# Performance work log

Measured on AMD Instinct MI355X. Metric: run time of the kernel, lower is better.

The kernel has to match this reference:

```python
import jax, jax.numpy as jnp
import numpy as np

B, S, D_IN, D_OUT = 4, 2048, 768, 768

def setup_inputs() -> dict:
    key = jax.random.key(0)
    kx, kq, kk, kv = jax.random.split(key, 4)
    scale = 1.0 / np.sqrt(D_IN)
    return {
        "x": jax.random.normal(kx, (B, S, D_IN), dtype=jnp.float32),
        "Wq": jax.random.normal(kq, (D_OUT, D_IN), dtype=jnp.float32) * scale,
        "Wk": jax.random.normal(kk, (D_OUT, D_IN), dtype=jnp.float32) * scale,
        "Wv": jax.random.normal(kv, (D_OUT, D_IN), dtype=jnp.float32) * scale,
    }

def reference(x, Wq, Wk, Wv):
    # torch Linear: y = x @ W.T  (W is [d_out, d_in])
    q = jnp.einsum('bsd,od->bso', x, Wq)
    k = jnp.einsum('bsd,od->bso', x, Wk)
    v = jnp.einsum('bsd,od->bso', x, Wv)
    scores = jnp.einsum('bqo,bko->bqk', q, k)  # [B,S,S]
    causal = jnp.tril(jnp.ones((scores.shape[1], scores.shape[2]), dtype=bool))
    neg_inf = jnp.array(-jnp.inf, dtype=scores.dtype)
    scores = jnp.where(causal, scores, neg_inf)
    inv_sqrt_d = jnp.asarray(1.0 / np.sqrt(q.shape[-1]), dtype=scores.dtype)
    weights = jax.nn.softmax(scores * inv_sqrt_d, axis=-1)
    # dropout p=0.0 -> identity
    return jnp.einsum('bqk,bko->bqo', weights, v)
```

## Files before the change

kernel.cpp:

```cpp
#include <hip/hip_runtime.h>
#include <hip/hip_bf16.h>
#include <cstdint>
#include <cstddef>


typedef __attribute__((ext_vector_type(8))) short short8;
typedef __attribute__((ext_vector_type(4))) float f32x4;

#define GPTR(p) (const __attribute__((address_space(1))) void*)(p)
#define LPTR(p) (__attribute__((address_space(3))) void*)(p)

constexpr int CB = 4, CS = 2048, CD = 768;
constexpr int CBS = CB * CS;

__device__ inline unsigned short f2bf_bits(float v) {
    __hip_bfloat16 h = __float2bfloat16(v);
    unsigned short u;
    __builtin_memcpy(&u, &h, 2);
    return u;
}

__device__ inline ushort4 cvt4(float4 f) {
    ushort4 u;
    u.x = f2bf_bits(f.x); u.y = f2bf_bits(f.y);
    u.z = f2bf_bits(f.z); u.w = f2bf_bits(f.w);
    return u;
}

__global__ __launch_bounds__(256) void cvt_all(
    const float4* __restrict__ x,  const float4* __restrict__ wq,
    const float4* __restrict__ wk, const float4* __restrict__ wv,
    ushort4* __restrict__ x16, ushort4* __restrict__ w16,
    float4* __restrict__ rsum4)
{
    constexpr int NX = CBS * CD / 4;
    constexpr int NW = CD * CD / 4;
    constexpr int NT = NX + 3 * NW;
    const int i = blockIdx.x * 256 + threadIdx.x;
    if (i < NX) {
        x16[i] = cvt4(x[i]);
    } else if (i < NT) {
        const int j = i - NX;
        if (j < NW)            w16[j] = cvt4(wq[j]);
        else if (j < 2 * NW)   w16[j] = cvt4(wk[j - NW]);
        else                   w16[j] = cvt4(wv[j - 2 * NW]);
    } else {
        const int j = i - NT;
        rsum4[j] = float4{0.f, 0.f, 0.f, 0.f};
    }
}

template <int BM>
__device__ __forceinline__ void gemm_core(
    const __hip_bfloat16* __restrict__ A,
    const __hip_bfloat16* __restrict__ B,
    __hip_bfloat16* As, __hip_bfloat16* Bs,
    int m0, int n0, int K, int kend,
    f32x4 (&acc)[BM / 32][4])
{
    constexpr int AC = BM / 16;
    constexpr int SC = AC + 8;
    constexpr int MI = BM / 32;

    const int t  = threadIdx.x;
    const int w  = t >> 6;
    const int l  = t & 63;
    const int lq = l >> 4;
    const int lm = l & 15;
    const int wm = (w >> 1) * (BM / 2);
    const int wn = (w & 1) * 64;

    const int srow = l >> 2;
    const int scol = (l & 3) * 8;

    auto stage = [&](int buf, int k0) {
#pragma unroll
        for (int ci = 0; ci < SC / 4; ++ci) {
            const int c = ci * 4 + w;
            if (c < AC) {
                __builtin_amdgcn_global_load_lds(
                    GPTR(A + (size_t)(m0 + c * 16 + srow) * K + k0 + scol),
                    LPTR(&As[buf * BM * 32 + c * 512]), 16, 0, 0);
            } else {
                const int c2 = c - AC;
                __builtin_amdgcn_global_load_lds(
                    GPTR(B + (size_t)(n0 + c2 * 16 + srow) * K + k0 + scol),
                    LPTR(&Bs[buf * 128 * 32 + c2 * 512]), 16, 0, 0);
            }
        }
    };

    stage(0, 0);
    asm volatile("s_waitcnt vmcnt(0)");
    __syncthreads();

    int cur = 0;
    for (int k0 = 0; k0 < kend; k0 += 32) {
        if (k0 + 32 < kend)
            stage(cur ^ 1, k0 + 32);

        short8 af[MI], bf[4];
#pragma unroll
        for (int i = 0; i < MI; ++i)
            af[i] = *(const short8*)&As[cur * BM * 32 + (wm + i * 16 + lm) * 32 + lq * 8];
#pragma unroll
        for (int j = 0; j < 4; ++j)
            bf[j] = *(const short8*)&Bs[cur * 128 * 32 + (wn + j * 16 + lm) * 32 + lq * 8];

#pragma unroll
        for (int i = 0; i < MI; ++i)
#pragma unroll
            for (int j = 0; j < 4; ++j)
                acc[i][j] = __builtin_amdgcn_mfma_f32_16x16x32_bf16(
                    af[i], bf[j], acc[i][j], 0, 0, 0);

        __syncthreads();
        cur ^= 1;
    }
}

template <int MI>
__device__ __forceinline__ void zero_acc(f32x4 (&acc)[MI][4]) {
#pragma unroll
    for (int i = 0; i < MI; ++i)
#pragma unroll
        for (int j = 0; j < 4; ++j)
            acc[i][j] = f32x4{0.f, 0.f, 0.f, 0.f};
}

__global__ __launch_bounds__(256) void qkv_gemm(
    const __hip_bfloat16* __restrict__ x16,
    const __hip_bfloat16* __restrict__ w16,
    __hip_bfloat16* __restrict__ q16,
    __hip_bfloat16* __restrict__ k16,
    __hip_bfloat16* __restrict__ vt16)
{
    __shared__ __align__(16) __hip_bfloat16 As[2 * 128 * 32];
    __shared__ __align__(16) __hip_bfloat16 Bs[2 * 128 * 32];

    const int t  = threadIdx.x;
    const int w  = t >> 6;
    const int l  = t & 63;
    const int lq = l >> 4;
    const int lm = l & 15;
    const int wm = (w >> 1) * 64;
    const int wn = (w & 1) * 64;

    f32x4 acc[4][4];
    zero_acc<4>(acc);

    const __hip_bfloat16* A;
    const __hip_bfloat16* B;
    __hip_bfloat16* C;
    int m0, n0, ldc;

    const int id = blockIdx.x;
    if (id < 768) {
        const int proj = id / 384;
        const int r    = id % 384;
        n0 = (r % 6) * 128;
        m0 = (r / 6) * 128;
        A = x16; B = w16 + (size_t)proj * CD * CD;
        C = proj ? k16 : q16; ldc = CD;
    } else {
        int r = id - 768;
        const int b  = r / 96;  r %= 96;
        n0 = (r % 16) * 128;
        m0 = (r / 16) * 128;
        A = w16 + (size_t)2 * CD * CD;
        B = x16  + (size_t)b * CS * CD;
        C = vt16 + (size_t)b * CD * CS; ldc = CS;
    }

    gemm_core<128>(A, B, As, Bs, m0, n0, CD, CD, acc);

#pragma unroll
    for (int i = 0; i < 4; ++i)
#pragma unroll
        for (int j = 0; j < 4; ++j) {
            const int n = n0 + wn + j * 16 + lm;
#pragma unroll
            for (int r = 0; r < 4; ++r) {
                const int m = m0 + wm + i * 16 + lq * 4 + r;
                C[(size_t)m * ldc + n] = __float2bfloat16(acc[i][j][r]);
            }
        }
}

__global__ __launch_bounds__(256) void scores_gemm(
    const __hip_bfloat16* __restrict__ q16,
    const __hip_bfloat16* __restrict__ k16,
    __hip_bfloat16* __restrict__ sp16,
    float* __restrict__ rowsum,
    float scale)
{
    const int g  = blockIdx.x;
    const int b  = g & 3;
    const int tt = g >> 2;
    int s = (int)sqrtf((float)tt);
    while ((s + 1) * (s + 1) <= tt) ++s;
    while (s * s > tt) --s;
    int mi, nj;
    if (tt < s * (s + 1)) { mi = 2 * s - 1; nj = tt - s * s; }
    else                  { mi = 2 * s;     nj = tt - s * (s + 1); }
    const int m0 = mi * 64;
    const int n0 = nj * 128;

    __shared__ __align__(16) __hip_bfloat16 As[2 * 64 * 32];
    __shared__ __align__(16) __hip_bfloat16 Bs[2 * 128 * 32];

    const __hip_bfloat16* A = q16 + (size_t)b * CS * CD;
    const __hip_bfloat16* B = k16 + (size_t)b * CS * CD;
    __hip_bfloat16* C = sp16 + (size_t)b * CS * CS;
    float* rs = rowsum + (size_t)b * CS;

    f32x4 acc[2][4];
    zero_acc<2>(acc);
    gemm_core<64>(A, B, As, Bs, m0, n0, CD, CD, acc);

    const int t  = threadIdx.x;
    const int w  = t >> 6;
    const int l  = t & 63;
    const int lq = l >> 4;
    const int lm = l & 15;
    const int wm = (w >> 1) * 32;
    const int wn = (w & 1) * 64;

#pragma unroll
    for (int i = 0; i < 2; ++i) {
        float psum[4] = {0.f, 0.f, 0.f, 0.f};
#pragma unroll
        for (int j = 0; j < 4; ++j) {
            const int n = n0 + wn + j * 16 + lm;
#pragma unroll
            for (int r = 0; r < 4; ++r) {
                const int m = m0 + wm + i * 16 + lq * 4 + r;
                float e = (n <= m) ? __expf(acc[i][j][r] * scale) : 0.f;
                C[(size_t)m * CS + n] = __float2bfloat16(e);
                psum[r] += e;
            }
        }
#pragma unroll
        for (int r = 0; r < 4; ++r) {
#pragma unroll
            for (int off = 1; off < 16; off <<= 1)
                psum[r] += __shfl_xor(psum[r], off);
            if (lm == 0) {
                const int m = m0 + wm + i * 16 + lq * 4 + r;
                atomicAdd(&rs[m], psum[r]);
            }
        }
    }
}

__global__ __launch_bounds__(256) void pv_gemm(
    const __hip_bfloat16* __restrict__ sp16,
    const __hip_bfloat16* __restrict__ vt16,
    const float* __restrict__ rowsum,
    float* __restrict__ out)
{
    const int id   = blockIdx.x;
    const int mrev = id / 24;
    int r          = id % 24;
    const int b    = r / 6;
    const int n0   = (r % 6) * 128;
    const int mi   = 31 - mrev;
    const int m0   = mi * 64;
    const int kend = m0 + 64;

    __shared__ __align__(16) __hip_bfloat16 As[2 * 64 * 32];
    __shared__ __align__(16) __hip_bfloat16 Bs[2 * 128 * 32];

    const __hip_bfloat16* A = sp16 + (size_t)b * CS * CS;
    const __hip_bfloat16* B = vt16 + (size_t)b * CD * CS;
    float* Co = out + (size_t)b * CS * CD;
    const float* rs = rowsum + (size_t)b * CS;

    f32x4 acc[2][4];
    zero_acc<2>(acc);
    gemm_core<64>(A, B, As, Bs, m0, n0, CS, kend, acc);

    const int t  = threadIdx.x;
    const int w  = t >> 6;
    const int l  = t & 63;
    const int lq = l >> 4;
    const int lm = l & 15;
    const int wm = (w >> 1) * 32;
    const int wn = (w & 1) * 64;

#pragma unroll
    for (int i = 0; i < 2; ++i) {
        float inv[4];
#pragma unroll
        for (int r2 = 0; r2 < 4; ++r2)
            inv[r2] = 1.0f / rs[m0 + wm + i * 16 + lq * 4 + r2];
#pragma unroll
        for (int j = 0; j < 4; ++j) {
            const int n = n0 + wn + j * 16 + lm;
#pragma unroll
            for (int r2 = 0; r2 < 4; ++r2) {
                const int m = m0 + wm + i * 16 + lq * 4 + r2;
                Co[(size_t)m * CD + n] = acc[i][j][r2] * inv[r2];
            }
        }
    }
}

extern "C" void kernel_launch(void* const* d_in, const int* in_sizes, int n_in,
                              void* d_out, int out_size, void* d_ws, size_t ws_size,
                              hipStream_t stream)
{
    const float* x  = (const float*)d_in[0];
    const float* Wq = (const float*)d_in[1];
    const float* Wk = (const float*)d_in[2];
    const float* Wv = (const float*)d_in[3];
    float* out = (float*)d_out;

    char* ws = (char*)d_ws;
    size_t off = 0;
    auto alloc = [&](size_t bytes) { char* p = ws + off; off += bytes; return p; };

    __hip_bfloat16* x16  = (__hip_bfloat16*)alloc((size_t)CBS * CD * 2);
    __hip_bfloat16* q16  = (__hip_bfloat16*)alloc((size_t)CBS * CD * 2);
    __hip_bfloat16* k16  = (__hip_bfloat16*)alloc((size_t)CBS * CD * 2);
    __hip_bfloat16* vt16 = (__hip_bfloat16*)alloc((size_t)CBS * CD * 2);
    __hip_bfloat16* sp16 = (__hip_bfloat16*)alloc((size_t)CB * CS * CS * 2);
    __hip_bfloat16* w16  = (__hip_bfloat16*)alloc((size_t)3 * CD * CD * 2);
    float*          rsum = (float*)alloc((size_t)CB * CS * sizeof(float));

    constexpr int NCVT_BLK = (CBS * CD + 3 * CD * CD) / 4 / 256 + 8;
    cvt_all<<<NCVT_BLK, 256, 0, stream>>>(
        (const float4*)x, (const float4*)Wq, (const float4*)Wk, (const float4*)Wv,
        (ushort4*)x16, (ushort4*)w16, (float4*)rsum);

    qkv_gemm<<<1152, 256, 0, stream>>>(x16, w16, q16, k16, vt16);

    scores_gemm<<<1088, 256, 0, stream>>>(
        q16, k16, sp16, rsum, 0.03608439182435161f);

    pv_gemm<<<768, 256, 0, stream>>>(sp16, vt16, rsum, out);
}
```

Baseline: 193.9 us.

## Use 256x256 tiled 8-wave GEMM core and move V projection into scores launch

Replaces the 128-tile GEMM core with a 256x256 tile, 512-thread kernel that uses XOR-swizzled LDS, a staged per-quarter prefetch pipeline and priority-raised MFMA phases. The Q/K projections get their own kernel, and the V^T projection now runs in the same launch as the causal scores GEMM so the two fill the GPU together. The aim is more data reuse per tile and better overlap of loads with MFMA work. In exchange, grids are much smaller (192 and 240 blocks), which risks poor CU occupancy and tail imbalance, and the causal diagonal tiles waste more work at this tile size.

```diff
diff --git a/kernel.cpp b/kernel.cpp
--- a/kernel.cpp
+++ b/kernel.cpp
@@ -9,6 +9,7 @@
 
 #define GPTR(p) (const __attribute__((address_space(1))) void*)(p)
 #define LPTR(p) (__attribute__((address_space(3))) void*)(p)
+#define MFMA16(a8, b8, c) c = __builtin_amdgcn_mfma_f32_16x16x32_bf16(a8, b8, c, 0, 0, 0)
 
 constexpr int CB = 4, CS = 2048, CD = 768;
 constexpr int CBS = CB * CS;
@@ -25,6 +26,15 @@
     u.x = f2bf_bits(f.x); u.y = f2bf_bits(f.y);
     u.z = f2bf_bits(f.z); u.w = f2bf_bits(f.w);
     return u;
+}
+
+template <int MI>
+__device__ __forceinline__ void zero_acc(f32x4 (&acc)[MI][4]) {
+#pragma unroll
+    for (int i = 0; i < MI; ++i)
+#pragma unroll
+        for (int j = 0; j < 4; ++j)
+            acc[i][j] = f32x4{0.f, 0.f, 0.f, 0.f};
 }
 
 __global__ __launch_bounds__(256) void cvt_all(
@@ -50,6 +60,279 @@
     }
 }
 
+__device__ __forceinline__ void gemm256_core(
+    const __hip_bfloat16* __restrict__ A,
+    const __hip_bfloat16* __restrict__ B,
+    __hip_bfloat16* As, __hip_bfloat16* Bs,
+    int m0, int n0, int K, int nkt,
+    f32x4 (&acc)[8][4])
+{
+    const int t   = threadIdx.x;
+    const int w   = t >> 6;
+    const int l   = t & 63;
+    const int lq  = l >> 4;
+    const int lm  = l & 15;
+    const int wm  = w >> 2;
+    const int wn  = w & 3;
+    const int lm7 = lm & 7;
+    const int c0  = (lq ^ lm7) << 3;
+    const int c1  = c0 ^ 32;
+
+    const int rr0   = t >> 3;
+    const int gp8   = (t & 7) << 3;
+    const int g8    = (((t & 7) ^ (rr0 & 7)) << 3);
+    const int rowBa = ((rr0 & 32) << 1) | (rr0 & 31);
+
+    const __hip_bfloat16* Aori = A + (size_t)m0 * K;
+    const __hip_bfloat16* Bori = B + (size_t)n0 * K;
+
+    auto stage = [&](int reg, int bufT, int kt) {
+        const int kc = kt * 64 + g8;
+        const __hip_bfloat16* s0;
+        __hip_bfloat16* d;
+        if (reg == 0) {
+            s0 = Aori + (size_t)rr0 * K + kc;
+            d  = As + bufT * 16384 + rr0 * 64 + gp8;
+        } else if (reg == 2) {
+            s0 = Aori + (size_t)(64 + rr0) * K + kc;
+            d  = As + bufT * 16384 + (64 + rr0) * 64 + gp8;
+        } else if (reg == 3) {
+            s0 = Bori + (size_t)rowBa * K + kc;
+            d  = Bs + bufT * 16384 + rowBa * 64 + gp8;
+        } else {
+            s0 = Bori + (size_t)(32 + rowBa) * K + kc;
+            d  = Bs + bufT * 16384 + (32 + rowBa) * 64 + gp8;
+        }
+        __builtin_amdgcn_global_load_lds(GPTR(s0), LPTR(d), 16, 0, 0);
+        __builtin_amdgcn_global_load_lds(GPTR(s0 + (size_t)128 * K), LPTR(d + 8192), 16, 0, 0);
+    };
+
+    stage(0, 0, 0); stage(1, 0, 0); stage(2, 0, 0); stage(3, 0, 0);
+    stage(0, 1, 1); stage(1, 1, 1); stage(2, 1, 1);
+    asm volatile("s_waitcnt vmcnt(6)" ::: "memory");
+    __builtin_amdgcn_s_barrier();
+
+    for (int kt = 0; kt < nkt; ++kt) {
+        const int buf = kt & 1;
+        const __hip_bfloat16* Ab = As + buf * 16384 + wm * 8192 + lm * 64;
+        const __hip_bfloat16* Bb = Bs + buf * 16384 + (wn >> 1) * 8192 + (wn & 1) * 4096 + lm * 64;
+        short8 af[4][2], bf[2][2];
+
+#pragma unroll
+        for (int i = 0; i < 4; ++i) {
+            af[i][0] = *(const short8*)&Ab[i * 1024 + c0];
+            af[i][1] = *(const short8*)&Ab[i * 1024 + c1];
+        }
+#pragma unroll
+        for (int j = 0; j < 2; ++j) {
+            bf[j][0] = *(const short8*)&Bb[j * 1024 + c0];
+            bf[j][1] = *(const short8*)&Bb[j * 1024 + c1];
+        }
+        if (kt + 1 < nkt) stage(3, buf ^ 1, kt + 1);
+        __builtin_amdgcn_s_barrier();
+        asm volatile("s_waitcnt lgkmcnt(0)" ::: "memory");
+        __builtin_amdgcn_sched_barrier(0);
+        __builtin_amdgcn_s_setprio(1);
+#pragma unroll
+        for (int i = 0; i < 4; ++i)
+#pragma unroll
+            for (int j = 0; j < 2; ++j) {
+                MFMA16(af[i][0], bf[j][0], acc[i][j]);
+                MFMA16(af[i][1], bf[j][1], acc[i][j]);
+            }
+        __builtin_amdgcn_s_setprio(0);
+        __builtin_amdgcn_s_barrier();
+
+#pragma unroll
+        for (int j = 0; j < 2; ++j) {
+            bf[j][0] = *(const short8*)&Bb[(2 + j) * 1024 + c0];
+            bf[j][1] = *(const short8*)&Bb[(2 + j) * 1024 + c1];
+        }
+        if (kt + 2 < nkt) stage(0, buf, kt + 2);
+        __builtin_amdgcn_s_barrier();
+        asm volatile("s_waitcnt lgkmcnt(0)" ::: "memory");
+        __builtin_amdgcn_sched_barrier(0);
+        __builtin_amdgcn_s_setprio(1);
+#pragma unroll
+        for (int i = 0; i < 4; ++i)
+#pragma unroll
+            for (int j = 0; j < 2; ++j) {
+                MFMA16(af[i][0], bf[j][0], acc[i][2 + j]);
+                MFMA16(af[i][1], bf[j][1], acc[i][2 + j]);
+            }
+        __builtin_amdgcn_s_setprio(0);
+        __builtin_amdgcn_s_barrier();
+
+#pragma unroll
+        for (int i = 0; i < 4; ++i) {
+            af[i][0] = *(const short8*)&Ab[(4 + i) * 1024 + c0];
+            af[i][1] = *(const short8*)&Ab[(4 + i) * 1024 + c1];
+        }
+        if (kt + 2 < nkt) stage(1, buf, kt + 2);
+        __builtin_amdgcn_s_barrier();
+        asm volatile("s_waitcnt lgkmcnt(0)" ::: "memory");
+        __builtin_amdgcn_sched_barrier(0);
+        __builtin_amdgcn_s_setprio(1);
+#pragma unroll
+        for (int i = 0; i < 4; ++i)
+#pragma unroll
+            for (int j = 0; j < 2; ++j) {
+                MFMA16(af[i][0], bf[j][0], acc[4 + i][2 + j]);
+                MFMA16(af[i][1], bf[j][1], acc[4 + i][2 + j]);
+            }
+        __builtin_amdgcn_s_setprio(0);
+        __builtin_amdgcn_s_barrier();
+
+#pragma unroll
+        for (int j = 0; j < 2; ++j) {
+            bf[j][0] = *(const short8*)&Bb[j * 1024 + c0];
+            bf[j][1] = *(const short8*)&Bb[j * 1024 + c1];
+        }
+        if (kt + 2 < nkt) stage(2, buf, kt + 2);
+        __builtin_amdgcn_s_barrier();
+        asm volatile("s_waitcnt lgkmcnt(0)" ::: "memory");
+        __builtin_amdgcn_sched_barrier(0);
+        __builtin_amdgcn_s_setprio(1);
+#pragma unroll
+        for (int i = 0; i < 4; ++i)
+#pragma unroll
+            for (int j = 0; j < 2; ++j) {
+                MFMA16(af[i][0], bf[j][0], acc[4 + i][j]);
+                MFMA16(af[i][1], bf[j][1], acc[4 + i][j]);
+            }
+        __builtin_amdgcn_s_setprio(0);
+        if (kt + 2 < nkt) {
+            asm volatile("s_waitcnt vmcnt(6)" ::: "memory");
+        } else if (kt + 1 < nkt) {
+            asm volatile("s_waitcnt vmcnt(0)" ::: "memory");
+        }
+        __builtin_amdgcn_s_barrier();
+    }
+}
+
+__global__ __launch_bounds__(512, 2) void qk256_gemm(
+    const __hip_bfloat16* __restrict__ x16,
+    const __hip_bfloat16* __restrict__ w16,
+    __hip_bfloat16* __restrict__ q16,
+    __hip_bfloat16* __restrict__ k16)
+{
+    __shared__ __align__(16) __hip_bfloat16 As[2 * 16384];
+    __shared__ __align__(16) __hip_bfloat16 Bs[2 * 16384];
+
+    const int id   = blockIdx.x;
+    const int mi   = id / 6;
+    const int r    = id % 6;
+    const int proj = r / 3;
+    const int nj   = r % 3;
+    const int m0 = mi * 256, n0 = nj * 256;
+
+    f32x4 acc[8][4];
+    zero_acc<8>(acc);
+    gemm256_core(x16, w16 + (size_t)proj * CD * CD, As, Bs, m0, n0, CD, CD / 64, acc);
+
+    __hip_bfloat16* C = proj ? k16 : q16;
+    const int t = threadIdx.x, w = t >> 6, l = t & 63, lq = l >> 4, lm = l & 15;
+    const int wm = w >> 2, wn = w & 3;
+#pragma unroll
+    for (int i = 0; i < 8; ++i)
+#pragma unroll
+        for (int j = 0; j < 4; ++j) {
+            const int n = n0 + wn * 64 + j * 16 + lm;
+#pragma unroll
+            for (int r2 = 0; r2 < 4; ++r2) {
+                const int m = m0 + wm * 128 + i * 16 + lq * 4 + r2;
+                C[(size_t)m * CD + n] = __float2bfloat16(acc[i][j][r2]);
+            }
+        }
+}
+
+__global__ __launch_bounds__(512, 2) void scores_vt_gemm(
+    const __hip_bfloat16* __restrict__ q16,
+    const __hip_bfloat16* __restrict__ k16,
+    const __hip_bfloat16* __restrict__ x16,
+    const __hip_bfloat16* __restrict__ w16,
+    __hip_bfloat16* __restrict__ sp16,
+    __hip_bfloat16* __restrict__ vt16,
+    float* __restrict__ rowsum,
+    float scale)
+{
+    __shared__ __align__(16) __hip_bfloat16 As[2 * 16384];
+    __shared__ __align__(16) __hip_bfloat16 Bs[2 * 16384];
+
+    const int id = blockIdx.x;
+    const __hip_bfloat16 *A, *B;
+    int m0, n0, b;
+    const bool is_sc = (id < 144);
+    if (is_sc) {
+        b = id / 36;
+        const int tt = id % 36;
+        int mi = (int)((sqrtf(8.f * tt + 1.f) - 1.f) * 0.5f);
+        while ((mi + 1) * (mi + 2) / 2 <= tt) ++mi;
+        while (mi * (mi + 1) / 2 > tt) --mi;
+        const int nj = tt - mi * (mi + 1) / 2;
+        m0 = mi * 256; n0 = nj * 256;
+        A = q16 + (size_t)b * CS * CD;
+        B = k16 + (size_t)b * CS * CD;
+    } else {
+        int r = id - 144;
+        b = r / 24; r %= 24;
+        m0 = (r >> 3) * 256;
+        n0 = (r & 7) * 256;
+        A = w16 + (size_t)2 * CD * CD;
+        B = x16 + (size_t)b * CS * CD;
+    }
+
+    f32x4 acc[8][4];
+    zero_acc<8>(acc);
+    gemm256_core(A, B, As, Bs, m0, n0, CD, CD / 64, acc);
+
+    const int t = threadIdx.x, w = t >> 6, l = t & 63, lq = l >> 4, lm = l & 15;
+    const int wm = w >> 2, wn = w & 3;
+
+    if (is_sc) {
+        __hip_bfloat16* C = sp16 + (size_t)b * CS * CS;
+        float* rs = rowsum + (size_t)b * CS;
+#pragma unroll
+        for (int i = 0; i < 8; ++i) {
+            float psum[4] = {0.f, 0.f, 0.f, 0.f};
+#pragma unroll
+            for (int j = 0; j < 4; ++j) {
+                const int n = n0 + wn * 64 + j * 16 + lm;
+#pragma unroll
+                for (int r2 = 0; r2 < 4; ++r2) {
+                    const int m = m0 + wm * 128 + i * 16 + lq * 4 + r2;
+                    float e = (n <= m) ? __expf(acc[i][j][r2] * scale) : 0.f;
+                    C[(size_t)m * CS + n] = __float2bfloat16(e);
+                    psum[r2] += e;
+                }
+            }
+#pragma unroll
+            for (int r2 = 0; r2 < 4; ++r2) {
+#pragma unroll
+                for (int off = 1; off < 16; off <<= 1)
+                    psum[r2] += __shfl_xor(psum[r2], off);
+                if (lm == 0) {
+                    const int m = m0 + wm * 128 + i * 16 + lq * 4 + r2;
+                    atomicAdd(&rs[m], psum[r2]);
+                }
+            }
+        }
+    } else {
+        __hip_bfloat16* C = vt16 + (size_t)b * CD * CS;
+#pragma unroll
+        for (int i = 0; i < 8; ++i)
+#pragma unroll
+            for (int j = 0; j < 4; ++j) {
+                const int n = n0 + wn * 64 + j * 16 + lm;
+#pragma unroll
+                for (int r2 = 0; r2 < 4; ++r2) {
+                    const int m = m0 + wm * 128 + i * 16 + lq * 4 + r2;
+                    C[(size_t)m * CS + n] = __float2bfloat16(acc[i][j][r2]);
+                }
+            }
+    }
+}
+
 template <int BM>
 __device__ __forceinline__ void gemm_core(
     const __hip_bfloat16* __restrict__ A,
@@ -91,7 +374,7 @@
     };
 
     stage(0, 0);
-    asm volatile("s_waitcnt vmcnt(0)");
+    asm volatile("s_waitcnt vmcnt(0)" ::: "memory");
     __syncthreads();
 
     int cur = 0;
@@ -116,140 +399,6 @@
 
         __syncthreads();
         cur ^= 1;
-    }
-}
-
-template <int MI>
-__device__ __forceinline__ void zero_acc(f32x4 (&acc)[MI][4]) {
-#pragma unroll
-    for (int i = 0; i < MI; ++i)
-#pragma unroll
-        for (int j = 0; j < 4; ++j)
-            acc[i][j] = f32x4{0.f, 0.f, 0.f, 0.f};
-}
-
-__global__ __launch_bounds__(256) void qkv_gemm(
-    const __hip_bfloat16* __restrict__ x16,
-    const __hip_bfloat16* __restrict__ w16,
-    __hip_bfloat16* __restrict__ q16,
-    __hip_bfloat16* __restrict__ k16,
-    __hip_bfloat16* __restrict__ vt16)
-{
-    __shared__ __align__(16) __hip_bfloat16 As[2 * 128 * 32];
-    __shared__ __align__(16) __hip_bfloat16 Bs[2 * 128 * 32];
-
-    const int t  = threadIdx.x;
-    const int w  = t >> 6;
-    const int l  = t & 63;
-    const int lq = l >> 4;
-    const int lm = l & 15;
-    const int wm = (w >> 1) * 64;
-    const int wn = (w & 1) * 64;
-
-    f32x4 acc[4][4];
-    zero_acc<4>(acc);
-
-    const __hip_bfloat16* A;
-    const __hip_bfloat16* B;
-    __hip_bfloat16* C;
-    int m0, n0, ldc;
-
-    const int id = blockIdx.x;
-    if (id < 768) {
-        const int proj = id / 384;
-        const int r    = id % 384;
-        n0 = (r % 6) * 128;
-        m0 = (r / 6) * 128;
-        A = x16; B = w16 + (size_t)proj * CD * CD;
-        C = proj ? k16 : q16; ldc = CD;
-    } else {
-        int r = id - 768;
-        const int b  = r / 96;  r %= 96;
-        n0 = (r % 16) * 128;
-        m0 = (r / 16) * 128;
-        A = w16 + (size_t)2 * CD * CD;
-        B = x16  + (size_t)b * CS * CD;
-        C = vt16 + (size_t)b * CD * CS; ldc = CS;
-    }
-
-    gemm_core<128>(A, B, As, Bs, m0, n0, CD, CD, acc);
-
-#pragma unroll
-    for (int i = 0; i < 4; ++i)
-#pragma unroll
-        for (int j = 0; j < 4; ++j) {
-            const int n = n0 + wn + j * 16 + lm;
-#pragma unroll
-            for (int r = 0; r < 4; ++r) {
-                const int m = m0 + wm + i * 16 + lq * 4 + r;
-                C[(size_t)m * ldc + n] = __float2bfloat16(acc[i][j][r]);
-            }
-        }
-}
-
-__global__ __launch_bounds__(256) void scores_gemm(
-    const __hip_bfloat16* __restrict__ q16,
-    const __hip_bfloat16* __restrict__ k16,
-    __hip_bfloat16* __restrict__ sp16,
-    float* __restrict__ rowsum,
-    float scale)
-{
-    const int g  = blockIdx.x;
-    const int b  = g & 3;
-    const int tt = g >> 2;
-    int s = (int)sqrtf((float)tt);
-    while ((s + 1) * (s + 1) <= tt) ++s;
-    while (s * s > tt) --s;
-    int mi, nj;
-    if (tt < s * (s + 1)) { mi = 2 * s - 1; nj = tt - s * s; }
-    else                  { mi = 2 * s;     nj = tt - s * (s + 1); }
-    const int m0 = mi * 64;
-    const int n0 = nj * 128;
-
-    __shared__ __align__(16) __hip_bfloat16 As[2 * 64 * 32];
-    __shared__ __align__(16) __hip_bfloat16 Bs[2 * 128 * 32];
-
-    const __hip_bfloat16* A = q16 + (size_t)b * CS * CD;
-    const __hip_bfloat16* B = k16 + (size_t)b * CS * CD;
-    __hip_bfloat16* C = sp16 + (size_t)b * CS * CS;
-    float* rs = rowsum + (size_t)b * CS;
-
-    f32x4 acc[2][4];
-    zero_acc<2>(acc);
-    gemm_core<64>(A, B, As, Bs, m0, n0, CD, CD, acc);
-
-    const int t  = threadIdx.x;
-    const int w  = t >> 6;
-    const int l  = t & 63;
-    const int lq = l >> 4;
-    const int lm = l & 15;
-    const int wm = (w >> 1) * 32;
-    const int wn = (w & 1) * 64;
-
-#pragma unroll
-    for (int i = 0; i < 2; ++i) {
-        float psum[4] = {0.f, 0.f, 0.f, 0.f};
-#pragma unroll
-        for (int j = 0; j < 4; ++j) {
-            const int n = n0 + wn + j * 16 + lm;
-#pragma unroll
-            for (int r = 0; r < 4; ++r) {
-                const int m = m0 + wm + i * 16 + lq * 4 + r;
-                float e = (n <= m) ? __expf(acc[i][j][r] * scale) : 0.f;
-                C[(size_t)m * CS + n] = __float2bfloat16(e);
-                psum[r] += e;
-            }
-        }
-#pragma unroll
-        for (int r = 0; r < 4; ++r) {
-#pragma unroll
-            for (int off = 1; off < 16; off <<= 1)
-                psum[r] += __shfl_xor(psum[r], off);
-            if (lm == 0) {
-                const int m = m0 + wm + i * 16 + lq * 4 + r;
-                atomicAdd(&rs[m], psum[r]);
-            }
-        }
     }
 }
 
@@ -333,10 +482,10 @@
         (const float4*)x, (const float4*)Wq, (const float4*)Wk, (const float4*)Wv,
         (ushort4*)x16, (ushort4*)w16, (float4*)rsum);
 
-    qkv_gemm<<<1152, 256, 0, stream>>>(x16, w16, q16, k16, vt16);
-
-    scores_gemm<<<1088, 256, 0, stream>>>(
-        q16, k16, sp16, rsum, 0.03608439182435161f);
+    qk256_gemm<<<192, 512, 0, stream>>>(x16, w16, q16, k16);
+
+    scores_vt_gemm<<<240, 512, 0, stream>>>(
+        q16, k16, x16, w16, sp16, vt16, rsum, 0.03608439182435161f);
 
     pv_gemm<<<768, 256, 0, stream>>>(sp16, vt16, rsum, out);
 }
```

Result: no change. 193.6 us (-0.1%).

## Move V-transpose projection into scores kernel, add XCD swizzle and 64-wide K steps

Applied to the files above, without the earlier changes.

Splits the QKV projection so only Q and K are computed first. The V^T projection now runs as extra 64-row tiles in the same launch as the causal scores kernel, which helps fill that launch's uneven triangular grid. Adds an XCD-aware block-index swizzle so neighbouring tiles land on the same chiplet for L2 reuse. Adds a 64-tile GEMM core that stages two 32-wide K slabs per iteration, halving barriers, and uses it for scores, V^T and PV at the cost of more LDS per block.

```diff
diff --git a/kernel.cpp b/kernel.cpp
--- a/kernel.cpp
+++ b/kernel.cpp
@@ -12,6 +12,10 @@
 
 constexpr int CB = 4, CS = 2048, CD = 768;
 constexpr int CBS = CB * CS;
+
+__device__ __forceinline__ int xcd_swz(int bid, int nwg) {
+    return (bid & 7) * (nwg >> 3) + (bid >> 3);
+}
 
 __device__ inline unsigned short f2bf_bits(float v) {
     __hip_bfloat16 h = __float2bfloat16(v);
@@ -25,6 +29,15 @@
     u.x = f2bf_bits(f.x); u.y = f2bf_bits(f.y);
     u.z = f2bf_bits(f.z); u.w = f2bf_bits(f.w);
     return u;
+}
+
+template <int MI>
+__device__ __forceinline__ void zero_acc(f32x4 (&acc)[MI][4]) {
+#pragma unroll
+    for (int i = 0; i < MI; ++i)
+#pragma unroll
+        for (int j = 0; j < 4; ++j)
+            acc[i][j] = f32x4{0.f, 0.f, 0.f, 0.f};
 }
 
 __global__ __launch_bounds__(256) void cvt_all(
@@ -91,7 +104,7 @@
     };
 
     stage(0, 0);
-    asm volatile("s_waitcnt vmcnt(0)");
+    asm volatile("s_waitcnt vmcnt(0)" ::: "memory");
     __syncthreads();
 
     int cur = 0;
@@ -119,25 +132,26 @@
     }
 }
 
-template <int MI>
-__device__ __forceinline__ void zero_acc(f32x4 (&acc)[MI][4]) {
-#pragma unroll
-    for (int i = 0; i < MI; ++i)
-#pragma unroll
-        for (int j = 0; j < 4; ++j)
-            acc[i][j] = f32x4{0.f, 0.f, 0.f, 0.f};
-}
-
-__global__ __launch_bounds__(256) void qkv_gemm(
+__global__ __launch_bounds__(256) void qk_gemm(
     const __hip_bfloat16* __restrict__ x16,
     const __hip_bfloat16* __restrict__ w16,
     __hip_bfloat16* __restrict__ q16,
-    __hip_bfloat16* __restrict__ k16,
-    __hip_bfloat16* __restrict__ vt16)
+    __hip_bfloat16* __restrict__ k16)
 {
     __shared__ __align__(16) __hip_bfloat16 As[2 * 128 * 32];
     __shared__ __align__(16) __hip_bfloat16 Bs[2 * 128 * 32];
 
+    const int id   = xcd_swz(blockIdx.x, 768);
+    const int proj = id / 384;
+    const int r    = id % 384;
+    const int n0   = (r % 6) * 128;
+    const int m0   = (r / 6) * 128;
+
+    f32x4 acc[4][4];
+    zero_acc<4>(acc);
+    gemm_core<128>(x16, w16 + (size_t)proj * CD * CD, As, Bs, m0, n0, CD, CD, acc);
+
+    __hip_bfloat16* C = proj ? k16 : q16;
     const int t  = threadIdx.x;
     const int w  = t >> 6;
     const int l  = t & 63;
@@ -145,78 +159,28 @@
     const int lm = l & 15;
     const int wm = (w >> 1) * 64;
     const int wn = (w & 1) * 64;
-
-    f32x4 acc[4][4];
-    zero_acc<4>(acc);
-
-    const __hip_bfloat16* A;
-    const __hip_bfloat16* B;
-    __hip_bfloat16* C;
-    int m0, n0, ldc;
-
-    const int id = blockIdx.x;
-    if (id < 768) {
-        const int proj = id / 384;
-        const int r    = id % 384;
-        n0 = (r % 6) * 128;
-        m0 = (r / 6) * 128;
-        A = x16; B = w16 + (size_t)proj * CD * CD;
-        C = proj ? k16 : q16; ldc = CD;
-    } else {
-        int r = id - 768;
-        const int b  = r / 96;  r %= 96;
-        n0 = (r % 16) * 128;
-        m0 = (r / 16) * 128;
-        A = w16 + (size_t)2 * CD * CD;
-        B = x16  + (size_t)b * CS * CD;
-        C = vt16 + (size_t)b * CD * CS; ldc = CS;
-    }
-
-    gemm_core<128>(A, B, As, Bs, m0, n0, CD, CD, acc);
-
 #pragma unroll
     for (int i = 0; i < 4; ++i)
 #pragma unroll
         for (int j = 0; j < 4; ++j) {
             const int n = n0 + wn + j * 16 + lm;
 #pragma unroll
-            for (int r = 0; r < 4; ++r) {
-                const int m = m0 + wm + i * 16 + lq * 4 + r;
-                C[(size_t)m * ldc + n] = __float2bfloat16(acc[i][j][r]);
-            }
-        }
-}
-
-__global__ __launch_bounds__(256) void scores_gemm(
-    const __hip_bfloat16* __restrict__ q16,
-    const __hip_bfloat16* __restrict__ k16,
-    __hip_bfloat16* __restrict__ sp16,
-    float* __restrict__ rowsum,
-    float scale)
-{
-    const int g  = blockIdx.x;
-    const int b  = g & 3;
-    const int tt = g >> 2;
-    int s = (int)sqrtf((float)tt);
-    while ((s + 1) * (s + 1) <= tt) ++s;
-    while (s * s > tt) --s;
-    int mi, nj;
-    if (tt < s * (s + 1)) { mi = 2 * s - 1; nj = tt - s * s; }
-    else                  { mi = 2 * s;     nj = tt - s * (s + 1); }
-    const int m0 = mi * 64;
-    const int n0 = nj * 128;
-
-    __shared__ __align__(16) __hip_bfloat16 As[2 * 64 * 32];
-    __shared__ __align__(16) __hip_bfloat16 Bs[2 * 128 * 32];
-
-    const __hip_bfloat16* A = q16 + (size_t)b * CS * CD;
-    const __hip_bfloat16* B = k16 + (size_t)b * CS * CD;
-    __hip_bfloat16* C = sp16 + (size_t)b * CS * CS;
-    float* rs = rowsum + (size_t)b * CS;
-
-    f32x4 acc[2][4];
-    zero_acc<2>(acc);
-    gemm_core<64>(A, B, As, Bs, m0, n0, CD, CD, acc);
+            for (int r2 = 0; r2 < 4; ++r2) {
+                const int m = m0 + wm + i * 16 + lq * 4 + r2;
+                C[(size_t)m * CD + n] = __float2bfloat16(acc[i][j][r2]);
+            }
+        }
+}
+
+__device__ __forceinline__ void gemm64_core(
+    const __hip_bfloat16* __restrict__ A,
+    const __hip_bfloat16* __restrict__ B,
+    __hip_bfloat16* As, __hip_bfloat16* Bs,
+    int m0, int n0, int K, int kend,
+    f32x4 (&acc)[2][4])
+{
+    constexpr int AC = 4;
+    constexpr int SC = AC + 8;
 
     const int t  = threadIdx.x;
     const int w  = t >> 6;
@@ -226,30 +190,153 @@
     const int wm = (w >> 1) * 32;
     const int wn = (w & 1) * 64;
 
-#pragma unroll
-    for (int i = 0; i < 2; ++i) {
-        float psum[4] = {0.f, 0.f, 0.f, 0.f};
-#pragma unroll
-        for (int j = 0; j < 4; ++j) {
-            const int n = n0 + wn + j * 16 + lm;
-#pragma unroll
-            for (int r = 0; r < 4; ++r) {
-                const int m = m0 + wm + i * 16 + lq * 4 + r;
-                float e = (n <= m) ? __expf(acc[i][j][r] * scale) : 0.f;
-                C[(size_t)m * CS + n] = __float2bfloat16(e);
-                psum[r] += e;
-            }
-        }
-#pragma unroll
-        for (int r = 0; r < 4; ++r) {
-#pragma unroll
-            for (int off = 1; off < 16; off <<= 1)
-                psum[r] += __shfl_xor(psum[r], off);
-            if (lm == 0) {
-                const int m = m0 + wm + i * 16 + lq * 4 + r;
-                atomicAdd(&rs[m], psum[r]);
-            }
-        }
+    const int srow = l >> 2;
+    const int scol = (l & 3) * 8;
+
+    auto stage = [&](int buf, int k0) {
+#pragma unroll
+        for (int ci = 0; ci < 2 * SC / 4; ++ci) {
+            const int c    = ci * 4 + w;
+            const int slab = (c >= SC) ? 1 : 0;
+            const int cc   = c - slab * SC;
+            const int kofs = k0 + slab * 32 + scol;
+            if (cc < AC) {
+                __builtin_amdgcn_global_load_lds(
+                    GPTR(A + (size_t)(m0 + cc * 16 + srow) * K + kofs),
+                    LPTR(&As[buf * 4096 + slab * 2048 + cc * 512]), 16, 0, 0);
+            } else {
+                const int c2 = cc - AC;
+                __builtin_amdgcn_global_load_lds(
+                    GPTR(B + (size_t)(n0 + c2 * 16 + srow) * K + kofs),
+                    LPTR(&Bs[buf * 8192 + slab * 4096 + c2 * 512]), 16, 0, 0);
+            }
+        }
+    };
+
+    stage(0, 0);
+    asm volatile("s_waitcnt vmcnt(0)" ::: "memory");
+    __syncthreads();
+
+    int cur = 0;
+    for (int k0 = 0; k0 < kend; k0 += 64) {
+        if (k0 + 64 < kend)
+            stage(cur ^ 1, k0 + 64);
+
+#pragma unroll
+        for (int kk = 0; kk < 2; ++kk) {
+            short8 af[2], bf[4];
+#pragma unroll
+            for (int i = 0; i < 2; ++i)
+                af[i] = *(const short8*)&As[cur * 4096 + kk * 2048 + (wm + i * 16 + lm) * 32 + lq * 8];
+#pragma unroll
+            for (int j = 0; j < 4; ++j)
+                bf[j] = *(const short8*)&Bs[cur * 8192 + kk * 4096 + (wn + j * 16 + lm) * 32 + lq * 8];
+#pragma unroll
+            for (int i = 0; i < 2; ++i)
+#pragma unroll
+                for (int j = 0; j < 4; ++j)
+                    acc[i][j] = __builtin_amdgcn_mfma_f32_16x16x32_bf16(
+                        af[i], bf[j], acc[i][j], 0, 0, 0);
+        }
+
+        __syncthreads();
+        cur ^= 1;
+    }
+}
+
+__global__ __launch_bounds__(256) void scores_vt_gemm(
+    const __hip_bfloat16* __restrict__ q16,
+    const __hip_bfloat16* __restrict__ k16,
+    const __hip_bfloat16* __restrict__ x16,
+    const __hip_bfloat16* __restrict__ w16,
+    __hip_bfloat16* __restrict__ sp16,
+    __hip_bfloat16* __restrict__ vt16,
+    float* __restrict__ rowsum,
+    float scale)
+{
+    __shared__ __align__(16) __hip_bfloat16 As[2 * 4096];
+    __shared__ __align__(16) __hip_bfloat16 Bs[2 * 8192];
+
+    const int id = xcd_swz(blockIdx.x, 1856);
+    const bool is_sc = (id < 1088);
+    const __hip_bfloat16 *A, *B;
+    int m0, n0, b;
+
+    if (is_sc) {
+        b = id & 3;
+        const int tt = id >> 2;
+        int s = (int)sqrtf((float)tt);
+        while ((s + 1) * (s + 1) <= tt) ++s;
+        while (s * s > tt) --s;
+        int mi, nj;
+        if (tt < s * (s + 1)) { mi = 2 * s - 1; nj = tt - s * s; }
+        else                  { mi = 2 * s;     nj = tt - s * (s + 1); }
+        m0 = mi * 64;
+        n0 = nj * 128;
+        A = q16 + (size_t)b * CS * CD;
+        B = k16 + (size_t)b * CS * CD;
+    } else {
+        int r = id - 1088;
+        b = r / 192; r %= 192;
+        m0 = (r / 16) * 64;
+        n0 = (r % 16) * 128;
+        A = w16 + (size_t)2 * CD * CD;
+        B = x16 + (size_t)b * CS * CD;
+    }
+
+    f32x4 acc[2][4];
+    zero_acc<2>(acc);
+    gemm64_core(A, B, As, Bs, m0, n0, CD, CD, acc);
+
+    const int t  = threadIdx.x;
+    const int w  = t >> 6;
+    const int l  = t & 63;
+    const int lq = l >> 4;
+    const int lm = l & 15;
+    const int wm = (w >> 1) * 32;
+    const int wn = (w & 1) * 64;
+
+    if (is_sc) {
+        __hip_bfloat16* C = sp16 + (size_t)b * CS * CS;
+        float* rs = rowsum + (size_t)b * CS;
+#pragma unroll
+        for (int i = 0; i < 2; ++i) {
+            float psum[4] = {0.f, 0.f, 0.f, 0.f};
+#pragma unroll
+            for (int j = 0; j < 4; ++j) {
+                const int n = n0 + wn + j * 16 + lm;
+#pragma unroll
+                for (int r2 = 0; r2 < 4; ++r2) {
+                    const int m = m0 + wm + i * 16 + lq * 4 + r2;
+                    float e = (n <= m) ? __expf(acc[i][j][r2] * scale) : 0.f;
+                    C[(size_t)m * CS + n] = __float2bfloat16(e);
+                    psum[r2] += e;
+                }
+            }
+#pragma unroll
+            for (int r2 = 0; r2 < 4; ++r2) {
+#pragma unroll
+                for (int off = 1; off < 16; off <<= 1)
+                    psum[r2] += __shfl_xor(psum[r2], off);
+                if (lm == 0) {
+                    const int m = m0 + wm + i * 16 + lq * 4 + r2;
+                    atomicAdd(&rs[m], psum[r2]);
+                }
+            }
+        }
+    } else {
+        __hip_bfloat16* C = vt16 + (size_t)b * CD * CS;
+#pragma unroll
+        for (int i = 0; i < 2; ++i)
+#pragma unroll
+            for (int j = 0; j < 4; ++j) {
+                const int n = n0 + wn + j * 16 + lm;
+#pragma unroll
+                for (int r2 = 0; r2 < 4; ++r2) {
+                    const int m = m0 + wm + i * 16 + lq * 4 + r2;
+                    C[(size_t)m * CS + n] = __float2bfloat16(acc[i][j][r2]);
+                }
+            }
     }
 }
 
@@ -268,8 +355,8 @@
     const int m0   = mi * 64;
     const int kend = m0 + 64;
 
-    __shared__ __align__(16) __hip_bfloat16 As[2 * 64 * 32];
-    __shared__ __align__(16) __hip_bfloat16 Bs[2 * 128 * 32];
+    __shared__ __align__(16) __hip_bfloat16 As[2 * 4096];
+    __shared__ __align__(16) __hip_bfloat16 Bs[2 * 8192];
 
     const __hip_bfloat16* A = sp16 + (size_t)b * CS * CS;
     const __hip_bfloat16* B = vt16 + (size_t)b * CD * CS;
@@ -278,7 +365,7 @@
 
     f32x4 acc[2][4];
     zero_acc<2>(acc);
-    gemm_core<64>(A, B, As, Bs, m0, n0, CS, kend, acc);
+    gemm64_core(A, B, As, Bs, m0, n0, CS, kend, acc);
 
     const int t  = threadIdx.x;
     const int w  = t >> 6;
@@ -333,10 +420,10 @@
         (const float4*)x, (const float4*)Wq, (const float4*)Wk, (const float4*)Wv,
         (ushort4*)x16, (ushort4*)w16, (float4*)rsum);
 
-    qkv_gemm<<<1152, 256, 0, stream>>>(x16, w16, q16, k16, vt16);
-
-    scores_gemm<<<1088, 256, 0, stream>>>(
-        q16, k16, sp16, rsum, 0.03608439182435161f);
+    qk_gemm<<<768, 256, 0, stream>>>(x16, w16, q16, k16);
+
+    scores_vt_gemm<<<1856, 256, 0, stream>>>(
+        q16, k16, x16, w16, sp16, vt16, rsum, 0.03608439182435161f);
 
     pv_gemm<<<768, 256, 0, stream>>>(sp16, vt16, rsum, out);
 }
```

Measured after the change: 195.1 us. No clear change (+0.6%).
